# Optimization experiments

Measured on AMD Instinct MI355X. Metric: run time of the kernel, lower is better.

## Reference

```python
import jax, jax.numpy as jnp
import numpy as np
import math

C = 256
GROUPS = 32
EPS = 1e-5

def setup_inputs() -> dict:
    key = jax.random.key(0)
    ks = jax.random.split(key, 11)
    B, H, W = 8, 64, 64
    s = 1.0 / math.sqrt(C)
    return {
        "x": jax.random.normal(ks[0], (B, C, H, W), dtype=jnp.float32),
        "gamma": jnp.ones((C,), jnp.float32),
        "beta": jnp.zeros((C,), jnp.float32),
        "wq": jax.random.normal(ks[1], (C, C), jnp.float32) * s,
        "bq": jnp.zeros((C,), jnp.float32),
        "wk": jax.random.normal(ks[2], (C, C), jnp.float32) * s,
        "bk": jnp.zeros((C,), jnp.float32),
        "wv": jax.random.normal(ks[3], (C, C), jnp.float32) * s,
        "bv": jnp.zeros((C,), jnp.float32),
        "wp": jax.random.normal(ks[4], (C, C), jnp.float32) * s,
        "bp": jnp.zeros((C,), jnp.float32),
    }

def _group_norm(x, gamma, beta):
    B, Cc, H, W = x.shape
    xg = x.reshape(B, GROUPS, Cc // GROUPS, H, W)
    mu = xg.mean(axis=(2, 3, 4), keepdims=True)
    var = xg.var(axis=(2, 3, 4), keepdims=True)
    xn = ((xg - mu) * jax.lax.rsqrt(var + EPS)).reshape(B, Cc, H, W)
    return xn * gamma[None, :, None, None] + beta[None, :, None, None]

def reference(x, gamma, beta, wq, bq, wk, bk, wv, bv, wp, bp):
    B, Cc, H, W = x.shape
    T = H * W
    h = _group_norm(x, gamma, beta)           # (B,C,H,W)
    hf = h.reshape(B, Cc, T)                  # (B,C,T)
    # 1x1 convs = per-pixel linear maps over channels
    q = jnp.einsum('oc,bct->bto', wq, hf) + bq           # (B,T,C)
    k = jnp.einsum('oc,bct->bot', wk, hf) + bk[:, None]  # (B,C,T)
    v = jnp.einsum('oc,bct->bto', wv, hf) + bv           # (B,T,C)
    scores = jnp.einsum('btc,bcs->bts', q, k) / math.sqrt(Cc)
    attn = jax.nn.softmax(scores, axis=-1)    # (B,T,T)
    z = jnp.einsum('bts,bsc->btc', attn, v)   # (B,T,C)
    zf = z.transpose(0, 2, 1)                 # (B,C,T)
    proj = jnp.einsum('oc,bct->bot', wp, zf) + bp[:, None]
    return x + proj.reshape(B, Cc, H, W)
```

## Files before the change

### kernel.cpp

```cpp
#include <hip/hip_runtime.h>


typedef unsigned short u16;
typedef unsigned char u8;
typedef __attribute__((ext_vector_type(8))) short short8;
typedef __attribute__((ext_vector_type(4))) float f32x4;

#define MFMA16(a, b, c) __builtin_amdgcn_mfma_f32_16x16x32_bf16((a), (b), (c), 0, 0, 0)
#define MFMA16F8(a, b, c) __builtin_amdgcn_mfma_f32_16x16x32_fp8_fp8((a), (b), (c), 0, 0, 0)

#define GLL16(g, l)                                                            \
  __builtin_amdgcn_global_load_lds(                                            \
      (const __attribute__((address_space(1))) void*)(g),                      \
      (__attribute__((address_space(3))) void*)(l), 16, 0, 0)

#define BAR_VM8()  asm volatile("s_waitcnt vmcnt(8)\n\ts_barrier" ::: "memory")
#define BAR_VM4()  asm volatile("s_waitcnt vmcnt(4)\n\ts_barrier" ::: "memory")
#define BAR_LGKM() asm volatile("s_waitcnt lgkmcnt(0)\n\ts_barrier" ::: "memory")

#define CVT_PK_BF16(dst, lo, hi)                                               \
  asm("v_cvt_pk_bf16_f32 %0, %1, %2" : "=v"(dst) : "v"(lo), "v"(hi))

__device__ __forceinline__ u16 f2bf(float f) {
  union { float f; unsigned u; } v; v.f = f;
  unsigned u = v.u;
  return (u16)((u + 0x7FFFu + ((u >> 16) & 1u)) >> 16);
}

__device__ __forceinline__ u8 f2fp8(float f) {
  int p = __builtin_amdgcn_cvt_pk_fp8_f32(f, f, 0, false);
  return (u8)(p & 0xff);
}

__global__ __launch_bounds__(256) void conv_w(const float* __restrict__ s0,
                                              const float* __restrict__ s1,
                                              const float* __restrict__ s2,
                                              const float* __restrict__ s3,
                                              u16* __restrict__ dst) {
  const int m = blockIdx.y;
  const float* s = (m == 0) ? s0 : (m == 1) ? s1 : (m == 2) ? s2 : s3;
  const int i = (blockIdx.x * 256 + threadIdx.x) * 4;
  float4 v = *(const float4*)(s + i);
  u16* d = dst + m * 65536 + i;
  d[0] = f2bf(v.x); d[1] = f2bf(v.y); d[2] = f2bf(v.z); d[3] = f2bf(v.w);
}

__global__ __launch_bounds__(256) void gn_stats(const float* __restrict__ x,
                                                float2* __restrict__ stats) {
  const int bg = blockIdx.x;
  const float* p = x + (long)bg * 32768;
  const int tid = threadIdx.x;
  float s = 0.f, ss = 0.f;
  #pragma unroll 8
  for (int i = 0; i < 32; ++i) {
    float4 v = *(const float4*)(p + tid * 4 + i * 1024);
    s  += v.x + v.y + v.z + v.w;
    ss += v.x * v.x + v.y * v.y + v.z * v.z + v.w * v.w;
  }
  for (int off = 32; off; off >>= 1) {
    s  += __shfl_down(s, off);
    ss += __shfl_down(ss, off);
  }
  __shared__ float2 red[4];
  if ((tid & 63) == 0) red[tid >> 6] = make_float2(s, ss);
  __syncthreads();
  if (tid == 0) {
    float S  = red[0].x + red[1].x + red[2].x + red[3].x;
    float SS = red[0].y + red[1].y + red[2].y + red[3].y;
    float mean = S * (1.f / 32768.f);
    float var  = SS * (1.f / 32768.f) - mean * mean;
    stats[bg] = make_float2(mean, rsqrtf(var + 1e-5f));
  }
}

__global__ __launch_bounds__(256) void gn_apply(const float* __restrict__ x,
                                                const float2* __restrict__ stats,
                                                const float* __restrict__ gamma,
                                                const float* __restrict__ beta,
                                                u16* __restrict__ h_t) {
  __shared__ float tile[64][65];
  const int tid = threadIdx.x;
  const int b = blockIdx.z, c0 = blockIdx.y * 64, t0 = blockIdx.x * 64;
  {
    const int ci = tid >> 2, tj0 = (tid & 3) * 16;
    const int c = c0 + ci;
    float2 st = stats[b * 32 + (c >> 3)];
    float gm = gamma[c] * st.y;
    float bt = beta[c] - st.x * gm;
    const float* xp = x + ((long)(b * 256 + c) * 4096 + t0 + tj0);
    #pragma unroll
    for (int i = 0; i < 4; ++i) {
      float4 v = *(const float4*)(xp + i * 4);
      tile[ci][tj0 + i * 4 + 0] = v.x * gm + bt;
      tile[ci][tj0 + i * 4 + 1] = v.y * gm + bt;
      tile[ci][tj0 + i * 4 + 2] = v.z * gm + bt;
      tile[ci][tj0 + i * 4 + 3] = v.w * gm + bt;
    }
  }
  __syncthreads();
  {
    const int tj = tid >> 2, ci0 = (tid & 3) * 16;
    u16* hp = h_t + ((long)(b * 4096 + t0 + tj) * 256 + c0 + ci0);
    uint4 o0, o1;
    CVT_PK_BF16(o0.x, tile[ci0 +  0][tj], tile[ci0 +  1][tj]);
    CVT_PK_BF16(o0.y, tile[ci0 +  2][tj], tile[ci0 +  3][tj]);
    CVT_PK_BF16(o0.z, tile[ci0 +  4][tj], tile[ci0 +  5][tj]);
    CVT_PK_BF16(o0.w, tile[ci0 +  6][tj], tile[ci0 +  7][tj]);
    CVT_PK_BF16(o1.x, tile[ci0 +  8][tj], tile[ci0 +  9][tj]);
    CVT_PK_BF16(o1.y, tile[ci0 + 10][tj], tile[ci0 + 11][tj]);
    CVT_PK_BF16(o1.z, tile[ci0 + 12][tj], tile[ci0 + 13][tj]);
    CVT_PK_BF16(o1.w, tile[ci0 + 14][tj], tile[ci0 + 15][tj]);
    *(uint4*)hp = o0;
    *(uint4*)(hp + 8) = o1;
  }
}

template <bool ROW_BIAS, bool RESID>
__global__ __launch_bounds__(256, 2) void gemm_bt(
    const u16* __restrict__ A, long strideAz, const u16* __restrict__ B,
    long strideBz, const float* __restrict__ bias, float scale,
    u16* __restrict__ outb, float* __restrict__ outf,
    const float* __restrict__ resid, long strideOz, int N) {
  __shared__ u16 a_lds[128 * 32];
  __shared__ u16 b_lds[128 * 32];
  const int tid = threadIdx.x, w = tid >> 6, l = tid & 63;
  const int l15 = l & 15, l4 = l >> 4;
  const int bz = blockIdx.z;
  A += bz * strideAz;
  B += bz * strideBz;
  const long obase = (long)bz * strideOz;
  const int m0 = blockIdx.y * 128, n0 = blockIdx.x * 128;
  const int wm = (w >> 1) * 64, wn = (w & 1) * 64;

  f32x4 acc[4][4];
  #pragma unroll
  for (int i = 0; i < 4; ++i)
    #pragma unroll
    for (int j = 0; j < 4; ++j) acc[i][j] = (f32x4)0.f;

  for (int kt = 0; kt < 8; ++kt) {
    const int k0 = kt * 32;
    __syncthreads();
    #pragma unroll
    for (int j = 0; j < 2; ++j) {
      const int r0 = (w * 2 + j) * 16;
      const int row = r0 + (l >> 2);
      const int sg = (l & 3) ^ (row & 3);
      GLL16(A + (long)(m0 + row) * 256 + k0 + sg * 8, a_lds + r0 * 32);
      GLL16(B + (long)(n0 + row) * 256 + k0 + sg * 8, b_lds + r0 * 32);
    }
    __syncthreads();
    short8 af[4], bf[4];
    #pragma unroll
    for (int t = 0; t < 4; ++t) {
      const int ra = wm + t * 16 + l15;
      af[t] = *(const short8*)(a_lds + ra * 32 + ((l4 ^ (ra & 3)) * 8));
      const int rb = wn + t * 16 + l15;
      bf[t] = *(const short8*)(b_lds + rb * 32 + ((l4 ^ (rb & 3)) * 8));
    }
    #pragma unroll
    for (int mt = 0; mt < 4; ++mt)
      #pragma unroll
      for (int nt = 0; nt < 4; ++nt) acc[mt][nt] = MFMA16(af[mt], bf[nt], acc[mt][nt]);
  }

  if (!ROW_BIAS) {
    float bv[4];
    #pragma unroll
    for (int nt = 0; nt < 4; ++nt) bv[nt] = bias[n0 + wn + nt * 16 + l15];
    #pragma unroll
    for (int mt = 0; mt < 4; ++mt)
      #pragma unroll
      for (int nt = 0; nt < 4; ++nt)
        #pragma unroll
        for (int r = 0; r < 4; ++r) {
          const int row = m0 + wm + mt * 16 + l4 * 4 + r;
          const int col = n0 + wn + nt * 16 + l15;
          outb[obase + (long)row * N + col] = f2bf((acc[mt][nt][r] + bv[nt]) * scale);
        }
  } else {
    float bm[4][4];
    #pragma unroll
    for (int mt = 0; mt < 4; ++mt)
      #pragma unroll
      for (int r = 0; r < 4; ++r) bm[mt][r] = bias[m0 + wm + mt * 16 + l4 * 4 + r];
    #pragma unroll
    for (int mt = 0; mt < 4; ++mt)
      #pragma unroll
      for (int nt = 0; nt < 4; ++nt)
        #pragma unroll
        for (int r = 0; r < 4; ++r) {
          const int row = m0 + wm + mt * 16 + l4 * 4 + r;
          const int col = n0 + wn + nt * 16 + l15;
          const long idx = obase + (long)row * N + col;
          float v = acc[mt][nt][r] + bm[mt][r];
          if (RESID) outf[idx] = v + resid[idx];
          else       outb[idx] = f2bf(v);
        }
  }
}

__global__ __launch_bounds__(256, 2) void gemm_qk(
    const u16* __restrict__ A, const u16* __restrict__ Bw,
    const float* __restrict__ bq, const float* __restrict__ bk,
    u8* __restrict__ Qs8, u8* __restrict__ Ks8) {
  __shared__ u16 a_lds[128 * 32];
  __shared__ u16 b_lds[128 * 32];
  const int tid = threadIdx.x, w = tid >> 6, l = tid & 63;
  const int l15 = l & 15, l4 = l >> 4;
  const int m0 = blockIdx.y * 128, n0 = blockIdx.x * 128;
  const int wm = (w >> 1) * 64, wn = (w & 1) * 64;

  f32x4 acc[4][4];
  #pragma unroll
  for (int i = 0; i < 4; ++i)
    #pragma unroll
    for (int j = 0; j < 4; ++j) acc[i][j] = (f32x4)0.f;

  for (int kt = 0; kt < 8; ++kt) {
    const int k0 = kt * 32;
    __syncthreads();
    #pragma unroll
    for (int j = 0; j < 2; ++j) {
      const int r0 = (w * 2 + j) * 16;
      const int row = r0 + (l >> 2);
      const int sg = (l & 3) ^ (row & 3);
      GLL16(A + (long)(m0 + row) * 256 + k0 + sg * 8, a_lds + r0 * 32);
      GLL16(Bw + (long)(n0 + row) * 256 + k0 + sg * 8, b_lds + r0 * 32);
    }
    __syncthreads();
    short8 af[4], bf[4];
    #pragma unroll
    for (int t = 0; t < 4; ++t) {
      const int ra = wm + t * 16 + l15;
      af[t] = *(const short8*)(a_lds + ra * 32 + ((l4 ^ (ra & 3)) * 8));
      const int rb = wn + t * 16 + l15;
      bf[t] = *(const short8*)(b_lds + rb * 32 + ((l4 ^ (rb & 3)) * 8));
    }
    #pragma unroll
    for (int mt = 0; mt < 4; ++mt)
      #pragma unroll
      for (int nt = 0; nt < 4; ++nt) acc[mt][nt] = MFMA16(af[mt], bf[nt], acc[mt][nt]);
  }

  const bool isQ = n0 < 256;
  u8* out = isQ ? Qs8 : Ks8;
  const float* bias = isQ ? bq : bk;
  const float osc = isQ ? 0.25f : 0.36067376022224085f;
  const int nc0 = n0 & 255;
  float bv[4];
  #pragma unroll
  for (int nt = 0; nt < 4; ++nt) bv[nt] = bias[nc0 + wn + nt * 16 + l15];
  #pragma unroll
  for (int mt = 0; mt < 4; ++mt)
    #pragma unroll
    for (int nt = 0; nt < 4; ++nt)
      #pragma unroll
      for (int r = 0; r < 4; ++r) {
        const int row = m0 + wm + mt * 16 + l4 * 4 + r;
        const int col = nc0 + wn + nt * 16 + l15;
        out[(long)row * 256 + col] = f2fp8((acc[mt][nt][r] + bv[nt]) * osc);
      }
}

__global__ __launch_bounds__(256, 2) void attn_kernel(
    const u8* __restrict__ Qs8, const u8* __restrict__ Ks8,
    const u16* __restrict__ Vt, u16* __restrict__ Z) {
  __shared__ u8  k_lds8[16384];
  __shared__ u16 v_lds[16384];
  __shared__ u16 p_lds[64 * 72];
  __shared__ float l_red[256];

  const int tid = threadIdx.x, w = tid >> 6, l = tid & 63;
  const int l15 = l & 15, l4 = l >> 4;
  const int bid = blockIdx.x;
  const int batch = bid & 7;
  const int qt = bid >> 3;
  const int ws0 = (w & 1) * 32, wq0 = (w >> 1) * 32, wcolO = (w & 1) * 128;
  const long qrow_base = (long)batch * 4096 + qt * 64;

  const u8*  kbase = Ks8 + (long)batch * 4096 * 256;
  const u16* vbase = Vt + (long)batch * 256 * 4096;

  long qf[2][8];
  {
    const u8* qp = Qs8 + (qrow_base + wq0) * 256;
    #pragma unroll
    for (int qt2 = 0; qt2 < 2; ++qt2)
      #pragma unroll
      for (int ks = 0; ks < 8; ++ks)
        qf[qt2][ks] = *(const long*)(qp + (qt2 * 16 + l15) * 256 + ks * 32 + l4 * 8);
  }

  const int cvv = 8 * w + (l >> 3);
  const int sgv = (l & 7) ^ (cvv & 7);

  f32x4 o_acc[2][8];
  #pragma unroll
  for (int mt = 0; mt < 2; ++mt)
    #pragma unroll
    for (int nt = 0; nt < 8; ++nt) o_acc[mt][nt] = (f32x4)0.f;
  float rs2[2] = {0.f, 0.f};

  #pragma unroll
  for (int j = 0; j < 4; ++j) {
    const int r0 = (j * 4 + w) * 4;
    const int row = r0 + (l >> 4);
    const int g = (l & 15) ^ (row & 15);
    GLL16(kbase + (long)row * 256 + g * 16, k_lds8 + r0 * 256);
  }
  #pragma unroll
  for (int j = 0; j < 8; ++j) {
    const int c0 = (j * 4 + w) * 8;
    GLL16(vbase + (long)(c0 + (l >> 3)) * 4096 + sgv * 8, v_lds + c0 * 64);
  }

  for (int st = 0; st < 64; ++st) {
    const int snn = ((st + 1) & 63) * 64;

    BAR_VM8();

    f32x4 sacc[2][2];
    #pragma unroll
    for (int i = 0; i < 2; ++i)
      #pragma unroll
      for (int j = 0; j < 2; ++j) sacc[i][j] = (f32x4)0.f;
    __builtin_amdgcn_s_setprio(1);
    #pragma unroll
    for (int ks = 0; ks < 8; ++ks) {
      long kf[2];
      #pragma unroll
      for (int st2 = 0; st2 < 2; ++st2) {
        const int row = ws0 + st2 * 16 + l15;
        const int g = (ks * 2 + (l4 >> 1)) ^ l15;
        kf[st2] = *(const long*)(k_lds8 + row * 256 + g * 16 + (l4 & 1) * 8);
      }
      #pragma unroll
      for (int st2 = 0; st2 < 2; ++st2)
        #pragma unroll
        for (int qt2 = 0; qt2 < 2; ++qt2)
          sacc[st2][qt2] = MFMA16F8(kf[st2], qf[qt2][ks], sacc[st2][qt2]);
    }
    __builtin_amdgcn_s_setprio(0);

    #pragma unroll
    for (int st2 = 0; st2 < 2; ++st2)
      #pragma unroll
      for (int qt2 = 0; qt2 < 2; ++qt2) {
        float e0 = __builtin_exp2f(sacc[st2][qt2][0]);
        float e1 = __builtin_exp2f(sacc[st2][qt2][1]);
        float e2 = __builtin_exp2f(sacc[st2][qt2][2]);
        float e3 = __builtin_exp2f(sacc[st2][qt2][3]);
        rs2[qt2] += (e0 + e1) + (e2 + e3);
        unsigned pw0, pw1;
        CVT_PK_BF16(pw0, e0, e1);
        CVT_PK_BF16(pw1, e2, e3);
        *(uint2*)(p_lds + (wq0 + qt2 * 16 + l15) * 72 + ws0 + st2 * 16 + l4 * 4) =
            make_uint2(pw0, pw1);
      }

    BAR_LGKM();

    #pragma unroll
    for (int j = 0; j < 4; ++j) {
      const int r0 = (j * 4 + w) * 4;
      const int row = r0 + (l >> 4);
      const int g = (l & 15) ^ (row & 15);
      GLL16(kbase + (long)(snn + row) * 256 + g * 16, k_lds8 + r0 * 256);
    }

    BAR_VM4();

    __builtin_amdgcn_s_setprio(1);
    #pragma unroll
    for (int ks2 = 0; ks2 < 2; ++ks2) {
      short8 pa[2];
      #pragma unroll
      for (int mt = 0; mt < 2; ++mt)
        pa[mt] = *(const short8*)(p_lds + (wq0 + mt * 16 + l15) * 72 + ks2 * 32 + l4 * 8);
      #pragma unroll
      for (int nt = 0; nt < 8; ++nt) {
        const int c = wcolO + nt * 16 + l15;
        const int gv = (ks2 * 4 + l4) ^ (c & 7);
        short8 vb = *(const short8*)(v_lds + c * 64 + gv * 8);
        #pragma unroll
        for (int mt = 0; mt < 2; ++mt) o_acc[mt][nt] = MFMA16(pa[mt], vb, o_acc[mt][nt]);
      }
    }
    __builtin_amdgcn_s_setprio(0);

    BAR_LGKM();

    #pragma unroll
    for (int j = 0; j < 8; ++j) {
      const int c0 = (j * 4 + w) * 8;
      GLL16(vbase + (long)(c0 + (l >> 3)) * 4096 + snn + sgv * 8, v_lds + c0 * 64);
    }
  }

  #pragma unroll
  for (int qt2 = 0; qt2 < 2; ++qt2) {
    float v = rs2[qt2];
    v += __shfl_xor(v, 16);
    v += __shfl_xor(v, 32);
    if (l4 == 0) l_red[w * 64 + wq0 + qt2 * 16 + l15] = v;
  }
  __syncthreads();
  if (tid < 64) {
    const int w0 = (tid >> 5) * 2;
    float t = l_red[w0 * 64 + tid] + l_red[(w0 + 1) * 64 + tid];
    l_red[tid] = 1.f / t;
  }
  __syncthreads();

  #pragma unroll
  for (int mt = 0; mt < 2; ++mt) {
    float inv[4];
    #pragma unroll
    for (int r = 0; r < 4; ++r) inv[r] = l_red[wq0 + mt * 16 + l4 * 4 + r];
    #pragma unroll
    for (int nt = 0; nt < 8; ++nt) {
      const int col = wcolO + nt * 16 + l15;
      #pragma unroll
      for (int r = 0; r < 4; ++r) {
        const long row = qrow_base + wq0 + mt * 16 + l4 * 4 + r;
        Z[row * 256 + col] = f2bf(o_acc[mt][nt][r] * inv[r]);
      }
    }
  }
}

extern "C" void kernel_launch(void* const* d_in, const int* in_sizes, int n_in,
                              void* d_out, int out_size, void* d_ws, size_t ws_size,
                              hipStream_t stream) {
  (void)in_sizes; (void)n_in; (void)out_size; (void)ws_size;
  const float* x     = (const float*)d_in[0];
  const float* gamma = (const float*)d_in[1];
  const float* beta  = (const float*)d_in[2];
  const float* wq    = (const float*)d_in[3];
  const float* bq    = (const float*)d_in[4];
  const float* wk    = (const float*)d_in[5];
  const float* bk    = (const float*)d_in[6];
  const float* wv    = (const float*)d_in[7];
  const float* bv    = (const float*)d_in[8];
  const float* wp    = (const float*)d_in[9];
  const float* bp    = (const float*)d_in[10];
  float* out = (float*)d_out;

  char* ws = (char*)d_ws;
  u16*    wb    = (u16*)(ws);
  float2* stats = (float2*)(ws + 524288);
  u16*    h_t   = (u16*)(ws + 526336);
  u8*     Qs8   = (u8*)(ws + 17303552);
  u8*     Ks8   = (u8*)(ws + 25692160);
  u16*    Vt    = (u16*)(ws + 34080768);
  u16*    Zb    = (u16*)(ws + 50857984);

  conv_w<<<dim3(64, 4), dim3(256), 0, stream>>>(wq, wk, wv, wp, wb);
  gn_stats<<<dim3(256), dim3(256), 0, stream>>>(x, stats);
  gn_apply<<<dim3(64, 4, 8), dim3(256), 0, stream>>>(x, stats, gamma, beta, h_t);

  const long sB = 4096L * 256L, sO = 256L * 4096L;
  gemm_qk<<<dim3(4, 256), dim3(256), 0, stream>>>(h_t, wb, bq, bk, Qs8, Ks8);
  gemm_bt<true, false><<<dim3(32, 2, 8), dim3(256), 0, stream>>>(
      wb + 2 * 65536, 0L, h_t, sB, bv, 1.0f, Vt, nullptr, nullptr, sO, 4096);

  attn_kernel<<<dim3(512), dim3(256), 0, stream>>>(Qs8, Ks8, Vt, Zb);

  gemm_bt<true, true><<<dim3(32, 2, 8), dim3(256), 0, stream>>>(
      wb + 3 * 65536, 0L, Zb, sB, bp, 1.0f, nullptr, out, x, sO, 4096);
}
```

Measured before the change: 290.5 us.

## Fuse weight conversion, group-norm stats and apply into one prep kernel

Replaces three launches (weight bf16 conversion, group-norm statistics, group-norm apply/transpose) with a single kernel. Weight-conversion blocks and per-(batch,group) blocks share one grid. Each group block computes its stats in shared memory and then normalizes and transposes its own 8 channels in 256-token chunks, so there is no separate stats buffer or extra launch. The cost is less parallelism in the apply phase: 256 blocks each loop over 16 chunks instead of 2048 small blocks. The 16-byte output stores are also strided by 256 channels.

```diff
diff --git a/kernel.cpp b/kernel.cpp
--- a/kernel.cpp
+++ b/kernel.cpp
@@ -32,24 +32,26 @@
   return (u8)(p & 0xff);
 }
 
-__global__ __launch_bounds__(256) void conv_w(const float* __restrict__ s0,
-                                              const float* __restrict__ s1,
-                                              const float* __restrict__ s2,
-                                              const float* __restrict__ s3,
-                                              u16* __restrict__ dst) {
-  const int m = blockIdx.y;
-  const float* s = (m == 0) ? s0 : (m == 1) ? s1 : (m == 2) ? s2 : s3;
-  const int i = (blockIdx.x * 256 + threadIdx.x) * 4;
-  float4 v = *(const float4*)(s + i);
-  u16* d = dst + m * 65536 + i;
-  d[0] = f2bf(v.x); d[1] = f2bf(v.y); d[2] = f2bf(v.z); d[3] = f2bf(v.w);
-}
-
-__global__ __launch_bounds__(256) void gn_stats(const float* __restrict__ x,
-                                                float2* __restrict__ stats) {
-  const int bg = blockIdx.x;
-  const float* p = x + (long)bg * 32768;
-  const int tid = threadIdx.x;
+__global__ __launch_bounds__(256) void prep(
+    const float* __restrict__ x,
+    const float* __restrict__ gamma, const float* __restrict__ beta,
+    const float* __restrict__ wq, const float* __restrict__ wk,
+    const float* __restrict__ wv, const float* __restrict__ wp,
+    u16* __restrict__ wb, u16* __restrict__ h_t) {
+  const int bid = blockIdx.x, tid = threadIdx.x;
+  if (bid < 256) {
+    const int m = bid >> 6;
+    const float* s = (m == 0) ? wq : (m == 1) ? wk : (m == 2) ? wv : wp;
+    const int i = ((bid & 63) * 256 + tid) * 4;
+    float4 v = *(const float4*)(s + i);
+    u16* d = wb + m * 65536 + i;
+    d[0] = f2bf(v.x); d[1] = f2bf(v.y); d[2] = f2bf(v.z); d[3] = f2bf(v.w);
+    return;
+  }
+  const int gid = bid - 256;
+  const int b = gid >> 5, g = gid & 31;
+  const float* p = x + (long)gid * 32768;
+
   float s = 0.f, ss = 0.f;
   #pragma unroll 8
   for (int i = 0; i < 32; ++i) {
@@ -62,6 +64,7 @@
     ss += __shfl_down(ss, off);
   }
   __shared__ float2 red[4];
+  __shared__ float2 stat;
   if ((tid & 63) == 0) red[tid >> 6] = make_float2(s, ss);
   __syncthreads();
   if (tid == 0) {
@@ -69,49 +72,44 @@
     float SS = red[0].y + red[1].y + red[2].y + red[3].y;
     float mean = S * (1.f / 32768.f);
     float var  = SS * (1.f / 32768.f) - mean * mean;
-    stats[bg] = make_float2(mean, rsqrtf(var + 1e-5f));
-  }
-}
-
-__global__ __launch_bounds__(256) void gn_apply(const float* __restrict__ x,
-                                                const float2* __restrict__ stats,
-                                                const float* __restrict__ gamma,
-                                                const float* __restrict__ beta,
-                                                u16* __restrict__ h_t) {
-  __shared__ float tile[64][65];
-  const int tid = threadIdx.x;
-  const int b = blockIdx.z, c0 = blockIdx.y * 64, t0 = blockIdx.x * 64;
-  {
-    const int ci = tid >> 2, tj0 = (tid & 3) * 16;
-    const int c = c0 + ci;
-    float2 st = stats[b * 32 + (c >> 3)];
-    float gm = gamma[c] * st.y;
-    float bt = beta[c] - st.x * gm;
-    const float* xp = x + ((long)(b * 256 + c) * 4096 + t0 + tj0);
-    #pragma unroll
-    for (int i = 0; i < 4; ++i) {
-      float4 v = *(const float4*)(xp + i * 4);
-      tile[ci][tj0 + i * 4 + 0] = v.x * gm + bt;
-      tile[ci][tj0 + i * 4 + 1] = v.y * gm + bt;
-      tile[ci][tj0 + i * 4 + 2] = v.z * gm + bt;
-      tile[ci][tj0 + i * 4 + 3] = v.w * gm + bt;
-    }
+    stat = make_float2(mean, rsqrtf(var + 1e-5f));
   }
   __syncthreads();
-  {
-    const int tj = tid >> 2, ci0 = (tid & 3) * 16;
-    u16* hp = h_t + ((long)(b * 4096 + t0 + tj) * 256 + c0 + ci0);
-    uint4 o0, o1;
-    CVT_PK_BF16(o0.x, tile[ci0 +  0][tj], tile[ci0 +  1][tj]);
-    CVT_PK_BF16(o0.y, tile[ci0 +  2][tj], tile[ci0 +  3][tj]);
-    CVT_PK_BF16(o0.z, tile[ci0 +  4][tj], tile[ci0 +  5][tj]);
-    CVT_PK_BF16(o0.w, tile[ci0 +  6][tj], tile[ci0 +  7][tj]);
-    CVT_PK_BF16(o1.x, tile[ci0 +  8][tj], tile[ci0 +  9][tj]);
-    CVT_PK_BF16(o1.y, tile[ci0 + 10][tj], tile[ci0 + 11][tj]);
-    CVT_PK_BF16(o1.z, tile[ci0 + 12][tj], tile[ci0 + 13][tj]);
-    CVT_PK_BF16(o1.w, tile[ci0 + 14][tj], tile[ci0 + 15][tj]);
-    *(uint4*)hp = o0;
-    *(uint4*)(hp + 8) = o1;
+  const float mean = stat.x, rstd = stat.y;
+
+  __shared__ float tile[8][257];
+  const int cr = tid >> 5;
+  const int c_g = g * 8;
+  const float gm = gamma[c_g + cr] * rstd;
+  const float bt = beta[c_g + cr] - mean * gm;
+  const float* xc = x + ((long)(b * 256 + c_g + cr) * 4096);
+  u16* hb = h_t + ((long)b * 4096) * 256 + c_g;
+
+  for (int ch = 0; ch < 16; ++ch) {
+    const int t0 = ch * 256;
+    {
+      const int tj = (tid & 31) * 8;
+      float4 v0 = *(const float4*)(xc + t0 + tj);
+      float4 v1 = *(const float4*)(xc + t0 + tj + 4);
+      tile[cr][tj + 0] = v0.x * gm + bt;
+      tile[cr][tj + 1] = v0.y * gm + bt;
+      tile[cr][tj + 2] = v0.z * gm + bt;
+      tile[cr][tj + 3] = v0.w * gm + bt;
+      tile[cr][tj + 4] = v1.x * gm + bt;
+      tile[cr][tj + 5] = v1.y * gm + bt;
+      tile[cr][tj + 6] = v1.z * gm + bt;
+      tile[cr][tj + 7] = v1.w * gm + bt;
+    }
+    __syncthreads();
+    {
+      uint4 o;
+      CVT_PK_BF16(o.x, tile[0][tid], tile[1][tid]);
+      CVT_PK_BF16(o.y, tile[2][tid], tile[3][tid]);
+      CVT_PK_BF16(o.z, tile[4][tid], tile[5][tid]);
+      CVT_PK_BF16(o.w, tile[6][tid], tile[7][tid]);
+      *(uint4*)(hb + (long)(t0 + tid) * 256) = o;
+    }
+    __syncthreads();
   }
 }
 
@@ -449,16 +447,14 @@
 
   char* ws = (char*)d_ws;
   u16*    wb    = (u16*)(ws);
-  float2* stats = (float2*)(ws + 524288);
   u16*    h_t   = (u16*)(ws + 526336);
   u8*     Qs8   = (u8*)(ws + 17303552);
   u8*     Ks8   = (u8*)(ws + 25692160);
   u16*    Vt    = (u16*)(ws + 34080768);
   u16*    Zb    = (u16*)(ws + 50857984);
 
-  conv_w<<<dim3(64, 4), dim3(256), 0, stream>>>(wq, wk, wv, wp, wb);
-  gn_stats<<<dim3(256), dim3(256), 0, stream>>>(x, stats);
-  gn_apply<<<dim3(64, 4, 8), dim3(256), 0, stream>>>(x, stats, gamma, beta, h_t);
+  prep<<<dim3(512), dim3(256), 0, stream>>>(x, gamma, beta, wq, wk, wv, wp,
+                                            wb, h_t);
 
   const long sB = 4096L * 256L, sO = 256L * 4096L;
   gemm_qk<<<dim3(4, 256), dim3(256), 0, stream>>>(h_t, wb, bq, bk, Qs8, Ks8);
```

Result: slower. 297.7 us (+2.4%).
